# Optimization experiments

Hardware: AMD Instinct MI355X
Metric: run time of the kernel (lower is better)

## Reference

```python
import jax, jax.numpy as jnp
import numpy as np


def squash(t, axis=-1):
    sq = jnp.sum(t * t, axis=axis, keepdims=True)
    scale = sq / (1.0 + sq)
    return scale * t / jnp.sqrt(sq + 1e-8)


def setup_inputs() -> dict:
    key = jax.random.key(0)
    k1, k2 = jax.random.split(key)
    B, in_caps, out_caps, in_dim, out_dim = 128, 2048, 32, 8, 16
    x = jax.random.normal(k1, (B, in_caps, in_dim), dtype=jnp.float32)
    W = jax.random.normal(k2, (in_caps, out_caps, in_dim, out_dim), dtype=jnp.float32)
    return {"x": x, "W": W}


def reference(x, W):
    # x: [B, in_caps, in_dim], W: [in_caps, out_caps, in_dim, out_dim]
    # u_hat: [B, in_caps, out_caps, out_dim]
    u_hat = jnp.einsum('bni,noid->bnod', x, W)
    B, in_caps, out_caps, _ = u_hat.shape
    b = jnp.zeros((B, in_caps, out_caps, 1), dtype=u_hat.dtype)
    v = None
    for i in range(3):
        c = jax.nn.softmax(b, axis=2)              # over out_caps
        s = jnp.sum(c * u_hat, axis=1)             # [B, out_caps, out_dim]
        v = squash(s)                              # [B, out_caps, out_dim]
        if i < 2:
            b = b + jnp.sum(u_hat * v[:, None], axis=-1, keepdims=True)
    return v
```

## Files before the change

kernel.cpp:

```cpp
#include <hip/hip_runtime.h>


constexpr int NC = 2048;
constexpr int OC = 32;
constexpr int OD = 16;

typedef const __attribute__((address_space(1))) void* gas1_t;
typedef __attribute__((address_space(3))) void* las3_t;

__device__ __forceinline__ void gld16(const void* g, void* l) {
    __builtin_amdgcn_global_load_lds((gas1_t)g, (las3_t)l, 16, 0, 0);
}

#define MEMFENCE() asm volatile("" ::: "memory")
#define BAR() do { MEMFENCE(); __builtin_amdgcn_s_barrier(); MEMFENCE(); } while (0)

__global__ __launch_bounds__(256)
void transpose_W(const float* __restrict__ Wg, float* __restrict__ Wtg)
{
    const float4* W4  = (const float4*)Wg;
    float4* Wt4 = (float4*)Wtg;
    const int n = blockIdx.x;
    const int tid = threadIdx.x;
#pragma unroll
    for (int j = 0; j < 4; ++j) {
        const int L  = j * 256 + tid;
        const int o  = L & 31;
        const int dq = (L >> 5) & 3;
        const int i  = L >> 7;
        Wt4[(size_t)n * 1024 + L] = W4[(size_t)n * 1024 + o * 32 + i * 4 + dq];
    }
}

template<bool FIRST>
__global__ __launch_bounds__(256)
__attribute__((amdgpu_waves_per_eu(3, 3)))
void caps_stream4(const float* __restrict__ xg, const float* __restrict__ Wtg,
                  const float* __restrict__ vin, float* __restrict__ pout)
{
    const int tid  = threadIdx.x;
    const int bid  = blockIdx.x;
    const int bt   = bid >> 7;
    const int nsup = bid & 127;
    const int w    = __builtin_amdgcn_readfirstlane(tid >> 6);
    const int lane = tid & 63;
    const int o    = lane & 31;
    const int h    = lane >> 5;
    const int b0   = bt * 16 + w * 4;
    const int nbase = nsup * 16;

    const float4* Wt4 = (const float4*)Wtg;

    float4 acc[4][2];
#pragma unroll
    for (int r = 0; r < 4; ++r)
#pragma unroll
        for (int qq = 0; qq < 2; ++qq) acc[r][qq] = make_float4(0.f, 0.f, 0.f, 0.f);

    float4 vr[4][2];
    if (!FIRST) {
        const float4* v4 = (const float4*)vin;
#pragma unroll
        for (int r = 0; r < 4; ++r)
#pragma unroll
            for (int qq = 0; qq < 2; ++qq)
                vr[r][qq] = v4[(size_t)(b0 + r) * 128 + o * 4 + h * 2 + qq];
    }

#pragma unroll 1
    for (int t = 0; t < 16; ++t) {
        const int n = nbase + t;

        float xs[4][8];
        {
            const float* xb = xg + ((size_t)b0 * NC + n) * 8;
#pragma unroll
            for (int r = 0; r < 4; ++r)
#pragma unroll
                for (int i = 0; i < 8; ++i) xs[r][i] = xb[(size_t)r * NC * 8 + i];
        }

        const float4* wn = Wt4 + (size_t)n * 1024 + h * 64 + o;

        float4 u[4][2];
#pragma unroll
        for (int r = 0; r < 4; ++r)
#pragma unroll
            for (int qq = 0; qq < 2; ++qq) u[r][qq] = make_float4(0.f, 0.f, 0.f, 0.f);

        float4 wA[2][2], wB[2][2];
#pragma unroll
        for (int j = 0; j < 2; ++j)
#pragma unroll
            for (int qq = 0; qq < 2; ++qq) wA[j][qq] = wn[j * 128 + qq * 32];

#pragma unroll
        for (int ip = 0; ip < 4; ++ip) {
            if (ip < 3) {
#pragma unroll
                for (int j = 0; j < 2; ++j)
#pragma unroll
                    for (int qq = 0; qq < 2; ++qq)
                        wB[j][qq] = wn[(ip * 2 + 2 + j) * 128 + qq * 32];
            }
#pragma unroll
            for (int j = 0; j < 2; ++j) {
                const int i = ip * 2 + j;
#pragma unroll
                for (int qq = 0; qq < 2; ++qq) {
                    const float4 wv = wA[j][qq];
#pragma unroll
                    for (int r = 0; r < 4; ++r) {
                        float4* dst = FIRST ? &acc[r][qq] : &u[r][qq];
                        dst->x = fmaf(xs[r][i], wv.x, dst->x);
                        dst->y = fmaf(xs[r][i], wv.y, dst->y);
                        dst->z = fmaf(xs[r][i], wv.z, dst->z);
                        dst->w = fmaf(xs[r][i], wv.w, dst->w);
                    }
                }
            }
#pragma unroll
            for (int j = 0; j < 2; ++j)
#pragma unroll
                for (int qq = 0; qq < 2; ++qq) wA[j][qq] = wB[j][qq];
        }

        if (!FIRST) {
#pragma unroll
            for (int r = 0; r < 4; ++r) {
                float tp = 0.f;
#pragma unroll
                for (int qq = 0; qq < 2; ++qq) {
                    tp = fmaf(u[r][qq].x, vr[r][qq].x, tp);
                    tp = fmaf(u[r][qq].y, vr[r][qq].y, tp);
                    tp = fmaf(u[r][qq].z, vr[r][qq].z, tp);
                    tp = fmaf(u[r][qq].w, vr[r][qq].w, tp);
                }
                const float tt = tp + __shfl_xor(tp, 32);
                const float e = __expf(tt);
                float Z = e;
                Z += __shfl_xor(Z, 1);
                Z += __shfl_xor(Z, 2);
                Z += __shfl_xor(Z, 4);
                Z += __shfl_xor(Z, 8);
                Z += __shfl_xor(Z, 16);
                const float c = e / Z;
#pragma unroll
                for (int qq = 0; qq < 2; ++qq) {
                    acc[r][qq].x = fmaf(c, u[r][qq].x, acc[r][qq].x);
                    acc[r][qq].y = fmaf(c, u[r][qq].y, acc[r][qq].y);
                    acc[r][qq].z = fmaf(c, u[r][qq].z, acc[r][qq].z);
                    acc[r][qq].w = fmaf(c, u[r][qq].w, acc[r][qq].w);
                }
            }
        }
    }

    const float sc = FIRST ? (1.0f / 32.0f) : 1.0f;
    float4* P4 = (float4*)pout;
#pragma unroll
    for (int r = 0; r < 4; ++r) {
        const size_t base = ((size_t)(nsup * 128 + b0 + r) * 4 + h * 2) * 32 + o;
#pragma unroll
        for (int qq = 0; qq < 2; ++qq) {
            float4 v;
            v.x = acc[r][qq].x * sc; v.y = acc[r][qq].y * sc;
            v.z = acc[r][qq].z * sc; v.w = acc[r][qq].w * sc;
            P4[base + (size_t)qq * 32] = v;
        }
    }
}

template<int NR, bool FIRST, bool ATOMIC>
__global__ __launch_bounds__(256)
void caps_pass(const float* __restrict__ xg, const float* __restrict__ Wg,
               const float* __restrict__ vin, float* __restrict__ pout)
{
    __shared__ float4 Wl[2][1024];

    constexpr int NSUPC = 2048 / NR;
    const int tid  = threadIdx.x;
    const int bid  = blockIdx.x;
    const int bt   = bid / NSUPC;
    const int nsup = bid % NSUPC;
    const int w    = __builtin_amdgcn_readfirstlane(tid >> 6);
    const int lane = tid & 63;
    const int o    = lane & 31;
    const int h    = lane >> 5;
    const int sw   = o & 7;
    const int b0   = bt * 16 + w * 4;
    const int nbase = nsup * NR;

    const float4* Wg4 = (const float4*)Wg;

    float4 acc[4][2];
#pragma unroll
    for (int r = 0; r < 4; ++r)
#pragma unroll
        for (int qq = 0; qq < 2; ++qq) acc[r][qq] = make_float4(0.f, 0.f, 0.f, 0.f);

    float4 vr[4][2];
    if (!FIRST) {
        const float4* v4 = (const float4*)vin;
#pragma unroll
        for (int r = 0; r < 4; ++r)
#pragma unroll
            for (int qq = 0; qq < 2; ++qq)
                vr[r][qq] = v4[(size_t)(b0 + r) * 128 + o * 4 + h * 2 + qq];
    }

#pragma unroll
    for (int j = 0; j < 4; ++j) {
        const int L = tid + 256 * j;
        const int oo = L >> 5, cc = L & 31;
        gld16(&Wg4[(size_t)nbase * 1024 + oo * 32 + (cc ^ (oo & 7))], &Wl[0][L]);
    }

#pragma unroll 1
    for (int t = 0; t < NR; ++t) {
        BAR();
        if (t + 1 < NR) {
#pragma unroll
            for (int j = 0; j < 4; ++j) {
                const int L = tid + 256 * j;
                const int oo = L >> 5, cc = L & 31;
                gld16(&Wg4[(size_t)(nbase + t + 1) * 1024 + oo * 32 + (cc ^ (oo & 7))],
                      &Wl[(t + 1) & 1][L]);
            }
            asm volatile("s_waitcnt vmcnt(4)" ::: "memory");
        } else {
            asm volatile("s_waitcnt vmcnt(0)" ::: "memory");
        }
        BAR();

        const int n = nbase + t;
        float xs[4][8];
#pragma unroll
        for (int r = 0; r < 4; ++r) {
            const float* xp = xg + ((size_t)(b0 + r) * NC + n) * 8;
#pragma unroll
            for (int i = 0; i < 8; ++i) xs[r][i] = xp[i];
        }
        const float4* wrow = &Wl[t & 1][o * 32];

        __builtin_amdgcn_s_setprio(1);
        if (FIRST) {
#pragma unroll
            for (int i = 0; i < 8; ++i)
#pragma unroll
                for (int qq = 0; qq < 2; ++qq) {
                    const float4 wv = wrow[(i * 4 + h * 2 + qq) ^ sw];
#pragma unroll
                    for (int r = 0; r < 4; ++r) {
                        acc[r][qq].x = fmaf(xs[r][i], wv.x, acc[r][qq].x);
                        acc[r][qq].y = fmaf(xs[r][i], wv.y, acc[r][qq].y);
                        acc[r][qq].z = fmaf(xs[r][i], wv.z, acc[r][qq].z);
                        acc[r][qq].w = fmaf(xs[r][i], wv.w, acc[r][qq].w);
                    }
                }
        } else {
            float4 u[4][2];
#pragma unroll
            for (int r = 0; r < 4; ++r)
#pragma unroll
                for (int qq = 0; qq < 2; ++qq) u[r][qq] = make_float4(0.f, 0.f, 0.f, 0.f);
#pragma unroll
            for (int i = 0; i < 8; ++i)
#pragma unroll
                for (int qq = 0; qq < 2; ++qq) {
                    const float4 wv = wrow[(i * 4 + h * 2 + qq) ^ sw];
#pragma unroll
                    for (int r = 0; r < 4; ++r) {
                        u[r][qq].x = fmaf(xs[r][i], wv.x, u[r][qq].x);
                        u[r][qq].y = fmaf(xs[r][i], wv.y, u[r][qq].y);
                        u[r][qq].z = fmaf(xs[r][i], wv.z, u[r][qq].z);
                        u[r][qq].w = fmaf(xs[r][i], wv.w, u[r][qq].w);
                    }
                }
#pragma unroll
            for (int r = 0; r < 4; ++r) {
                float tp = 0.f;
#pragma unroll
                for (int qq = 0; qq < 2; ++qq) {
                    tp = fmaf(u[r][qq].x, vr[r][qq].x, tp);
                    tp = fmaf(u[r][qq].y, vr[r][qq].y, tp);
                    tp = fmaf(u[r][qq].z, vr[r][qq].z, tp);
                    tp = fmaf(u[r][qq].w, vr[r][qq].w, tp);
                }
                const float tt = tp + __shfl_xor(tp, 32);
                const float e = __expf(tt);
                float Z = e;
                Z += __shfl_xor(Z, 1);
                Z += __shfl_xor(Z, 2);
                Z += __shfl_xor(Z, 4);
                Z += __shfl_xor(Z, 8);
                Z += __shfl_xor(Z, 16);
                const float c = e / Z;
#pragma unroll
                for (int qq = 0; qq < 2; ++qq) {
                    acc[r][qq].x = fmaf(c, u[r][qq].x, acc[r][qq].x);
                    acc[r][qq].y = fmaf(c, u[r][qq].y, acc[r][qq].y);
                    acc[r][qq].z = fmaf(c, u[r][qq].z, acc[r][qq].z);
                    acc[r][qq].w = fmaf(c, u[r][qq].w, acc[r][qq].w);
                }
            }
        }
        __builtin_amdgcn_s_setprio(0);
    }

    const float sc = FIRST ? (1.0f / 32.0f) : 1.0f;
    if (ATOMIC) {
#pragma unroll
        for (int r = 0; r < 4; ++r) {
            float* sb = pout + (size_t)(b0 + r) * (OC * OD) + o * OD + h * 8;
#pragma unroll
            for (int qq = 0; qq < 2; ++qq) {
                atomicAdd(sb + qq * 4 + 0, acc[r][qq].x * sc);
                atomicAdd(sb + qq * 4 + 1, acc[r][qq].y * sc);
                atomicAdd(sb + qq * 4 + 2, acc[r][qq].z * sc);
                atomicAdd(sb + qq * 4 + 3, acc[r][qq].w * sc);
            }
        }
    } else {
        float4* P4 = (float4*)pout;
#pragma unroll
        for (int r = 0; r < 4; ++r) {
            const size_t base = ((size_t)(nsup * 128 + b0 + r) * 4 + h * 2) * 32 + o;
#pragma unroll
            for (int qq = 0; qq < 2; ++qq) {
                float4 v;
                v.x = acc[r][qq].x * sc; v.y = acc[r][qq].y * sc;
                v.z = acc[r][qq].z * sc; v.w = acc[r][qq].w * sc;
                P4[base + (size_t)qq * 32] = v;
            }
        }
    }
}

template<int NS>
__global__ void reduce_squash(const float* __restrict__ P, const float* __restrict__ vprev,
                              float* __restrict__ vout)
{
    __shared__ float sqb[256];
    const int tid = threadIdx.x;
    const int blk = blockIdx.x;
    const float4* P4 = (const float4*)P;

    float4 a = make_float4(0.f, 0.f, 0.f, 0.f);
#pragma unroll 8
    for (int ns = 0; ns < NS; ++ns) {
        const float4 p = P4[(size_t)ns * 16384 + blk * 256 + tid];
        a.x += p.x; a.y += p.y; a.z += p.z; a.w += p.w;
    }
    sqb[tid] = a.x * a.x + a.y * a.y + a.z * a.z + a.w * a.w;
    __syncthreads();
    const int base = tid & 0x9F;
    const float sq = sqb[base] + sqb[base + 32] + sqb[base + 64] + sqb[base + 96];
    const float f = sq / ((1.0f + sq) * sqrtf(sq + 1e-8f));

    const int b  = blk * 2 + (tid >> 7);
    const int hq = (tid >> 5) & 3;
    const int o  = tid & 31;
    const size_t unit = (size_t)(b * 32 + o) * 4 + hq;
    float4 r;
    r.x = a.x * f; r.y = a.y * f; r.z = a.z * f; r.w = a.w * f;
    if (vprev) {
        const float4 p = ((const float4*)vprev)[unit];
        r.x += p.x; r.y += p.y; r.z += p.z; r.w += p.w;
    }
    ((float4*)vout)[unit] = r;
}

__global__ void squash_k(const float* __restrict__ s, const float* __restrict__ vprev,
                         float* __restrict__ vout)
{
    const int row = blockIdx.x * blockDim.x + threadIdx.x;
    if (row >= 128 * 32) return;
    const float4* s4 = (const float4*)s;
    float4 t[4];
    float sq = 0.f;
#pragma unroll
    for (int q = 0; q < 4; ++q) {
        t[q] = s4[row * 4 + q];
        sq += t[q].x * t[q].x + t[q].y * t[q].y + t[q].z * t[q].z + t[q].w * t[q].w;
    }
    const float f = sq / ((1.0f + sq) * sqrtf(sq + 1e-8f));
    float4* o4 = (float4*)vout;
#pragma unroll
    for (int q = 0; q < 4; ++q) {
        float4 r;
        r.x = t[q].x * f; r.y = t[q].y * f; r.z = t[q].z * f; r.w = t[q].w * f;
        if (vprev) {
            const float4 p = ((const float4*)vprev)[row * 4 + q];
            r.x += p.x; r.y += p.y; r.z += p.z; r.w += p.w;
        }
        o4[row * 4 + q] = r;
    }
}

extern "C" void kernel_launch(void* const* d_in, const int* in_sizes, int n_in,
                              void* d_out, int out_size, void* d_ws, size_t ws_size,
                              hipStream_t stream)
{
    const float* x = (const float*)d_in[0];
    const float* W = (const float*)d_in[1];
    float* out = (float*)d_out;

    const size_t WT = (size_t)2048 * 32 * 128;
    const size_t P1 = (size_t)128 * 128 * 512;
    const size_t NEED1 = (WT + P1 + 2 * 65536) * sizeof(float);
    const size_t NEED2 = (P1 + 2 * 65536) * sizeof(float);

    if (ws_size >= NEED1) {
        float* Wt = (float*)d_ws;
        float* P  = Wt + WT;
        float* v0 = P + P1;
        float* vs = v0 + 65536;

        transpose_W<<<dim3(2048), dim3(256), 0, stream>>>(W, Wt);

        caps_stream4<true><<<dim3(1024), dim3(256), 0, stream>>>(x, Wt, nullptr, P);
        reduce_squash<128><<<dim3(64), dim3(256), 0, stream>>>(P, nullptr, v0);

        caps_stream4<false><<<dim3(1024), dim3(256), 0, stream>>>(x, Wt, v0, P);
        reduce_squash<128><<<dim3(64), dim3(256), 0, stream>>>(P, v0, vs);

        caps_stream4<false><<<dim3(1024), dim3(256), 0, stream>>>(x, Wt, vs, P);
        reduce_squash<128><<<dim3(64), dim3(256), 0, stream>>>(P, nullptr, out);
    } else if (ws_size >= NEED2) {
        float* P  = (float*)d_ws;
        float* v0 = P + P1;
        float* vs = v0 + 65536;

        caps_pass<16, true, false><<<dim3(1024), dim3(256), 0, stream>>>(x, W, nullptr, P);
        reduce_squash<128><<<dim3(64), dim3(256), 0, stream>>>(P, nullptr, v0);

        caps_pass<16, false, false><<<dim3(1024), dim3(256), 0, stream>>>(x, W, v0, P);
        reduce_squash<128><<<dim3(64), dim3(256), 0, stream>>>(P, v0, vs);

        caps_pass<16, false, false><<<dim3(1024), dim3(256), 0, stream>>>(x, W, vs, P);
        reduce_squash<128><<<dim3(64), dim3(256), 0, stream>>>(P, nullptr, out);
    } else {
        float* s  = (float*)d_ws;
        float* v0 = s + 65536;
        float* vs = v0 + 65536;
        const size_t sbytes = (size_t)65536 * sizeof(float);

        hipMemsetAsync(s, 0, sbytes, stream);
        caps_pass<16, true, true><<<dim3(1024), dim3(256), 0, stream>>>(x, W, nullptr, s);
        squash_k<<<dim3(16), dim3(256), 0, stream>>>(s, nullptr, v0);

        hipMemsetAsync(s, 0, sbytes, stream);
        caps_pass<16, false, true><<<dim3(1024), dim3(256), 0, stream>>>(x, W, v0, s);
        squash_k<<<dim3(16), dim3(256), 0, stream>>>(s, v0, vs);

        hipMemsetAsync(s, 0, sbytes, stream);
        caps_pass<16, false, true><<<dim3(1024), dim3(256), 0, stream>>>(x, W, vs, s);
        squash_k<<<dim3(16), dim3(256), 0, stream>>>(s, nullptr, out);
    }
}
```

Before: 188.7 us.

## Give each lane full out_dim for two batches instead of half-dim for four

```diff
diff --git a/kernel.cpp b/kernel.cpp
--- a/kernel.cpp
+++ b/kernel.cpp
@@ -35,8 +35,8 @@
 template<bool FIRST>
 __global__ __launch_bounds__(256)
 __attribute__((amdgpu_waves_per_eu(3, 3)))
-void caps_stream4(const float* __restrict__ xg, const float* __restrict__ Wtg,
-                  const float* __restrict__ vin, float* __restrict__ pout)
+void caps_stream_fd(const float* __restrict__ xg, const float* __restrict__ Wtg,
+                    const float* __restrict__ vin, float* __restrict__ pout)
 {
     const int tid  = threadIdx.x;
     const int bid  = blockIdx.x;
@@ -45,112 +45,102 @@
     const int w    = __builtin_amdgcn_readfirstlane(tid >> 6);
     const int lane = tid & 63;
     const int o    = lane & 31;
-    const int h    = lane >> 5;
+    const int rh   = lane >> 5;
     const int b0   = bt * 16 + w * 4;
+    const int bl   = b0 + rh * 2;
     const int nbase = nsup * 16;
 
     const float4* Wt4 = (const float4*)Wtg;
 
-    float4 acc[4][2];
-#pragma unroll
-    for (int r = 0; r < 4; ++r)
-#pragma unroll
-        for (int qq = 0; qq < 2; ++qq) acc[r][qq] = make_float4(0.f, 0.f, 0.f, 0.f);
-
-    float4 vr[4][2];
+    float4 acc[2][4];
+#pragma unroll
+    for (int j = 0; j < 2; ++j)
+#pragma unroll
+        for (int dq = 0; dq < 4; ++dq) acc[j][dq] = make_float4(0.f, 0.f, 0.f, 0.f);
+
+    float4 vr[2][4];
     if (!FIRST) {
         const float4* v4 = (const float4*)vin;
 #pragma unroll
-        for (int r = 0; r < 4; ++r)
-#pragma unroll
-            for (int qq = 0; qq < 2; ++qq)
-                vr[r][qq] = v4[(size_t)(b0 + r) * 128 + o * 4 + h * 2 + qq];
+        for (int j = 0; j < 2; ++j)
+#pragma unroll
+            for (int dq = 0; dq < 4; ++dq)
+                vr[j][dq] = v4[(size_t)(bl + j) * 128 + o * 4 + dq];
     }
 
 #pragma unroll 1
     for (int t = 0; t < 16; ++t) {
         const int n = nbase + t;
 
-        float xs[4][8];
-        {
-            const float* xb = xg + ((size_t)b0 * NC + n) * 8;
-#pragma unroll
-            for (int r = 0; r < 4; ++r)
-#pragma unroll
-                for (int i = 0; i < 8; ++i) xs[r][i] = xb[(size_t)r * NC * 8 + i];
-        }
-
-        const float4* wn = Wt4 + (size_t)n * 1024 + h * 64 + o;
-
-        float4 u[4][2];
-#pragma unroll
-        for (int r = 0; r < 4; ++r)
-#pragma unroll
-            for (int qq = 0; qq < 2; ++qq) u[r][qq] = make_float4(0.f, 0.f, 0.f, 0.f);
-
-        float4 wA[2][2], wB[2][2];
+        float xs[2][8];
+#pragma unroll
+        for (int j = 0; j < 2; ++j) {
+            const float4* xp = (const float4*)xg + ((size_t)(bl + j) * NC + n) * 2;
+            const float4 xa = xp[0];
+            const float4 xb = xp[1];
+            xs[j][0] = xa.x; xs[j][1] = xa.y; xs[j][2] = xa.z; xs[j][3] = xa.w;
+            xs[j][4] = xb.x; xs[j][5] = xb.y; xs[j][6] = xb.z; xs[j][7] = xb.w;
+        }
+
+        const float4* wn = Wt4 + (size_t)n * 1024 + o;
+
+        float4 u[2][4];
 #pragma unroll
         for (int j = 0; j < 2; ++j)
 #pragma unroll
-            for (int qq = 0; qq < 2; ++qq) wA[j][qq] = wn[j * 128 + qq * 32];
-
-#pragma unroll
-        for (int ip = 0; ip < 4; ++ip) {
-            if (ip < 3) {
-#pragma unroll
-                for (int j = 0; j < 2; ++j)
-#pragma unroll
-                    for (int qq = 0; qq < 2; ++qq)
-                        wB[j][qq] = wn[(ip * 2 + 2 + j) * 128 + qq * 32];
-            }
+            for (int dq = 0; dq < 4; ++dq) u[j][dq] = make_float4(0.f, 0.f, 0.f, 0.f);
+
+        float4 wA[4], wB[4];
+#pragma unroll
+        for (int dq = 0; dq < 4; ++dq) wA[dq] = wn[dq * 32];
+
+#pragma unroll
+        for (int i = 0; i < 8; ++i) {
+            if (i < 7) {
+#pragma unroll
+                for (int dq = 0; dq < 4; ++dq) wB[dq] = wn[((i + 1) * 4 + dq) * 32];
+            }
+#pragma unroll
+            for (int dq = 0; dq < 4; ++dq) {
+                const float4 wv = wA[dq];
+#pragma unroll
+                for (int j = 0; j < 2; ++j) {
+                    float4* dst = FIRST ? &acc[j][dq] : &u[j][dq];
+                    dst->x = fmaf(xs[j][i], wv.x, dst->x);
+                    dst->y = fmaf(xs[j][i], wv.y, dst->y);
+                    dst->z = fmaf(xs[j][i], wv.z, dst->z);
+                    dst->w = fmaf(xs[j][i], wv.w, dst->w);
+                }
+            }
+#pragma unroll
+            for (int dq = 0; dq < 4; ++dq) wA[dq] = wB[dq];
+        }
+
+        if (!FIRST) {
 #pragma unroll
             for (int j = 0; j < 2; ++j) {
-                const int i = ip * 2 + j;
-#pragma unroll
-                for (int qq = 0; qq < 2; ++qq) {
-                    const float4 wv = wA[j][qq];
-#pragma unroll
-                    for (int r = 0; r < 4; ++r) {
-                        float4* dst = FIRST ? &acc[r][qq] : &u[r][qq];
-                        dst->x = fmaf(xs[r][i], wv.x, dst->x);
-                        dst->y = fmaf(xs[r][i], wv.y, dst->y);
-                        dst->z = fmaf(xs[r][i], wv.z, dst->z);
-                        dst->w = fmaf(xs[r][i], wv.w, dst->w);
-                    }
-                }
-            }
-#pragma unroll
-            for (int j = 0; j < 2; ++j)
-#pragma unroll
-                for (int qq = 0; qq < 2; ++qq) wA[j][qq] = wB[j][qq];
-        }
-
-        if (!FIRST) {
-#pragma unroll
-            for (int r = 0; r < 4; ++r) {
                 float tp = 0.f;
 #pragma unroll
-                for (int qq = 0; qq < 2; ++qq) {
-                    tp = fmaf(u[r][qq].x, vr[r][qq].x, tp);
-                    tp = fmaf(u[r][qq].y, vr[r][qq].y, tp);
-                    tp = fmaf(u[r][qq].z, vr[r][qq].z, tp);
-                    tp = fmaf(u[r][qq].w, vr[r][qq].w, tp);
-                }
-                const float tt = tp + __shfl_xor(tp, 32);
-                const float e = __expf(tt);
+                for (int dq = 0; dq < 4; ++dq) {
+                    tp = fmaf(u[j][dq].x, vr[j][dq].x, tp);
+                    tp = fmaf(u[j][dq].y, vr[j][dq].y, tp);
+                    tp = fmaf(u[j][dq].z, vr[j][dq].z, tp);
+                    tp = fmaf(u[j][dq].w, vr[j][dq].w, tp);
+                }
+                const float e = __expf(tp);
                 float Z = e;
                 Z += __shfl_xor(Z, 1);
                 Z += __shfl_xor(Z, 2);
                 Z += __shfl_xor(Z, 4);
                 Z += __shfl_xor(Z, 8);
                 Z += __shfl_xor(Z, 16);
-                const float c = e / Z;
-#pragma unroll
-                for (int qq = 0; qq < 2; ++qq) {
-                    acc[r][qq].x = fmaf(c, u[r][qq].x, acc[r][qq].x);
-                    acc[r][qq].y = fmaf(c, u[r][qq].y, acc[r][qq].y);
-                    acc[r][qq].z = fmaf(c, u[r][qq].z, acc[r][qq].z);
-                    acc[r][qq].w = fmaf(c, u[r][qq].w, acc[r][qq].w);
+                const float c = e * __builtin_amdgcn_rcpf(Z);
+#pragma unroll
+                for (int dq = 0; dq < 4; ++dq) {
+                    acc[j][dq].x = fmaf(c, u[j][dq].x, acc[j][dq].x);
+                    acc[j][dq].y = fmaf(c, u[j][dq].y, acc[j][dq].y);
+                    acc[j][dq].z = fmaf(c, u[j][dq].z, acc[j][dq].z);
+                    acc[j][dq].w = fmaf(c, u[j][dq].w, acc[j][dq].w);
                 }
             }
         }
@@ -159,14 +149,14 @@
     const float sc = FIRST ? (1.0f / 32.0f) : 1.0f;
     float4* P4 = (float4*)pout;
 #pragma unroll
-    for (int r = 0; r < 4; ++r) {
-        const size_t base = ((size_t)(nsup * 128 + b0 + r) * 4 + h * 2) * 32 + o;
-#pragma unroll
-        for (int qq = 0; qq < 2; ++qq) {
+    for (int j = 0; j < 2; ++j) {
+        const size_t base = (size_t)(nsup * 128 + bl + j) * 4 * 32 + o;
+#pragma unroll
+        for (int dq = 0; dq < 4; ++dq) {
             float4 v;
-            v.x = acc[r][qq].x * sc; v.y = acc[r][qq].y * sc;
-            v.z = acc[r][qq].z * sc; v.w = acc[r][qq].w * sc;
-            P4[base + (size_t)qq * 32] = v;
+            v.x = acc[j][dq].x * sc; v.y = acc[j][dq].y * sc;
+            v.z = acc[j][dq].z * sc; v.w = acc[j][dq].w * sc;
+            P4[base + (size_t)dq * 32] = v;
         }
     }
 }
@@ -419,13 +409,13 @@
 
         transpose_W<<<dim3(2048), dim3(256), 0, stream>>>(W, Wt);
 
-        caps_stream4<true><<<dim3(1024), dim3(256), 0, stream>>>(x, Wt, nullptr, P);
+        caps_stream_fd<true><<<dim3(1024), dim3(256), 0, stream>>>(x, Wt, nullptr, P);
         reduce_squash<128><<<dim3(64), dim3(256), 0, stream>>>(P, nullptr, v0);
 
-        caps_stream4<false><<<dim3(1024), dim3(256), 0, stream>>>(x, Wt, v0, P);
+        caps_stream_fd<false><<<dim3(1024), dim3(256), 0, stream>>>(x, Wt, v0, P);
         reduce_squash<128><<<dim3(64), dim3(256), 0, stream>>>(P, v0, vs);
 
-        caps_stream4<false><<<dim3(1024), dim3(256), 0, stream>>>(x, Wt, vs, P);
+        caps_stream_fd<false><<<dim3(1024), dim3(256), 0, stream>>>(x, Wt, vs, P);
         reduce_squash<128><<<dim3(64), dim3(256), 0, stream>>>(P, nullptr, out);
     } else if (ws_size >= NEED2) {
         float* P  = (float*)d_ws;
```

New measurement: 285.8 us. +51.4%, slower.
